# Kernel tuning notes

Hardware: AMD Instinct MI355X
Metric: run time of the kernel (lower is better)

The kernel has to match this reference:

```python
import jax, jax.numpy as jnp
import numpy as np

ODE_UNFOLDS = 6
EPS = 1e-8


def setup_inputs() -> dict:
    key = jax.random.key(0)
    ks = jax.random.split(key, 16)
    B, T, IN, U = 256, 128, 64, 256

    def unif(k, shape, lo, hi):
        return jax.random.uniform(k, shape, jnp.float32, lo, hi)

    def pm1(k, shape):  # random +/-1 reversal potentials (as in ncps erev init)
        return (2.0 * jax.random.bernoulli(k, 0.5, shape) - 1.0).astype(jnp.float32)

    return {
        "x_ltc": jax.random.normal(ks[0], (B, T, IN), jnp.float32),
        "timespans": jnp.ones((B, T, 1), jnp.float32),
        # sensory synapses (input -> units)
        "sensory_mu": unif(ks[1], (IN, U), 0.3, 0.8),
        "sensory_sigma": unif(ks[2], (IN, U), 3.0, 8.0),
        "sensory_w": unif(ks[3], (IN, U), 0.001, 1.0),
        "sensory_erev": pm1(ks[4], (IN, U)),
        # recurrent synapses (units -> units)
        "mu": unif(ks[5], (U, U), 0.3, 0.8),
        "sigma": unif(ks[6], (U, U), 3.0, 8.0),
        "w": unif(ks[7], (U, U), 0.001, 1.0),
        "erev": pm1(ks[8], (U, U)),
        # per-neuron leak / capacitance
        "gleak": unif(ks[9], (U,), 0.001, 1.0),
        "vleak": unif(ks[10], (U,), -0.2, 0.2),
        "cm": unif(ks[11], (U,), 0.4, 0.6),
        # affine input / output mappings
        "input_w": jnp.ones((IN,), jnp.float32),
        "input_b": jnp.zeros((IN,), jnp.float32),
        "output_w": jnp.ones((U,), jnp.float32),
        "output_b": jnp.zeros((U,), jnp.float32),
        # head: Linear(hidden, 1)
        "head_w": jax.random.normal(ks[12], (1, U), jnp.float32) * 0.05,
        "head_b": jnp.zeros((1,), jnp.float32),
    }


def reference(x_ltc, timespans, sensory_mu, sensory_sigma, sensory_w, sensory_erev,
              mu, sigma, w, erev, gleak, vleak, cm,
              input_w, input_b, output_w, output_b, head_w, head_b):
    B = x_ltc.shape[0]
    U = gleak.shape[0]

    def gate(v, mu_, sigma_):
        # v: (B, pre) -> (B, pre, post) sigmoid activation
        return jax.nn.sigmoid(sigma_ * (v[:, :, None] - mu_))

    def cell(v, xt, elapsed):
        x = xt * input_w + input_b                              # (B, IN)
        s_act = sensory_w * gate(x, sensory_mu, sensory_sigma)  # (B, IN, U)
        w_num_s = jnp.sum(s_act * sensory_erev, axis=1)          # (B, U)
        w_den_s = jnp.sum(s_act, axis=1)                         # (B, U)
        cm_t = cm / (elapsed / ODE_UNFOLDS)                      # (B, U) via (B,1) bcast
        for _ in range(ODE_UNFOLDS):                             # semi-implicit Euler unfolds
            w_act = w * gate(v, mu, sigma)                       # (B, U, U)
            w_num = jnp.sum(w_act * erev, axis=1) + w_num_s
            w_den = jnp.sum(w_act, axis=1) + w_den_s
            num = cm_t * v + gleak * vleak + w_num
            den = cm_t + gleak + w_den
            v = num / (den + EPS)
        return v

    def step(v, inp):
        xt, el = inp
        return cell(v, xt, el), None

    v0 = jnp.zeros((B, U), x_ltc.dtype)
    xs = (jnp.swapaxes(x_ltc, 0, 1), jnp.swapaxes(timespans, 0, 1))  # (T,B,IN), (T,B,1)
    vT, _ = jax.lax.scan(step, v0, xs)
    h_out = vT * output_w + output_b                             # output mapping of last step
    return h_out @ head_w.T + head_b                             # (B, 1)
```

## Files before the change

### kernel.cpp

```cpp
#include <hip/hip_runtime.h>
#include <hip/hip_bf16.h>
#include <hip/hip_fp16.h>

#define LOG2E 1.4426950408889634f

constexpr int B_ = 256, T_ = 128, IN_ = 64, U_ = 256;
constexpr int UNFOLDS = 6;

constexpr size_t OFF_RCD = 0;
constexpr size_t OFF_RWS = 262144;
constexpr size_t OFF_SCD = 393216;
constexpr size_t OFF_SWS = 458752;
constexpr size_t OFF_ELF = 491520;
constexpr size_t OFF_VEC = 622592;

typedef _Float16 hv2 __attribute__((ext_vector_type(2)));

__device__ __forceinline__ float ldf(const void* p, int idx, bool isbf) {
  return isbf ? __bfloat162float(((const __hip_bfloat16*)p)[idx])
              : ((const float*)p)[idx];
}

__device__ __forceinline__ float fdot2f(__half2 a, __half2 b, float c) {
#if __has_builtin(__builtin_amdgcn_fdot2)
  return __builtin_amdgcn_fdot2(__builtin_bit_cast(hv2, a),
                                __builtin_bit_cast(hv2, b), c, false);
#else
  return c + __low2float(a) * __low2float(b) +
         __high2float(a) * __high2float(b);
#endif
}

__device__ __forceinline__ unsigned packpair(float lo, float hi) {
  return __builtin_bit_cast(unsigned, __builtin_amdgcn_cvt_pkrtz(lo, hi));
}

__global__ __launch_bounds__(256) void ltc_prep(
    const void* tspan, const void* smu, const void* ssigma, const void* sw,
    const void* serev, const void* mu, const void* sigma, const void* w,
    const void* erev, const void* gleak, const void* vleak, const void* cm,
    const void* inw, const void* inb, const void* outw, const void* outb,
    const void* headw, const void* headb, char* __restrict__ ws) {
  const bool isbf = (((const unsigned*)tspan)[0] == 0x3F803F80u);
  const int idx = blockIdx.x * blockDim.x + threadIdx.x;

  uint2*    rcd = (uint2*)(ws + OFF_RCD);
  unsigned* rws = (unsigned*)(ws + OFF_RWS);
  uint2*    scd = (uint2*)(ws + OFF_SCD);
  unsigned* sws = (unsigned*)(ws + OFF_SWS);
  float*    elf = (float*)(ws + OFF_ELF);
  float*    vec = (float*)(ws + OFF_VEC);

  if (idx < (U_ * U_) / 2) {
    const int j = idx & 255, P = idx >> 8;
    const int e0 = (2 * P) * U_ + j, e1 = (2 * P + 1) * U_ + j;
    float sg0 = ldf(sigma, e0, isbf), m0 = ldf(mu, e0, isbf);
    float w0  = ldf(w, e0, isbf),     er0 = ldf(erev, e0, isbf);
    float sg1 = ldf(sigma, e1, isbf), m1 = ldf(mu, e1, isbf);
    float w1  = ldf(w, e1, isbf),     er1 = ldf(erev, e1, isbf);
    __half2 C, D, W;
    C.x = __float2half_rn(sg0 * m0 * LOG2E);  C.y = __float2half_rn(sg1 * m1 * LOG2E);
    D.x = __float2half_rn(-sg0 * LOG2E);      D.y = __float2half_rn(-sg1 * LOG2E);
    W.x = __float2half_rn(w0 * er0);          W.y = __float2half_rn(w1 * er1);
    rcd[P * 256 + j] = make_uint2(__builtin_bit_cast(unsigned, C),
                                  __builtin_bit_cast(unsigned, D));
    rws[P * 256 + j] = __builtin_bit_cast(unsigned, W);
  }
  if (idx < (IN_ * U_) / 2) {
    const int j = idx & 255, P = idx >> 8;
    const int e0 = (2 * P) * U_ + j, e1 = (2 * P + 1) * U_ + j;
    float sg0 = ldf(ssigma, e0, isbf), m0 = ldf(smu, e0, isbf);
    float w0  = ldf(sw, e0, isbf),     er0 = ldf(serev, e0, isbf);
    float sg1 = ldf(ssigma, e1, isbf), m1 = ldf(smu, e1, isbf);
    float w1  = ldf(sw, e1, isbf),     er1 = ldf(serev, e1, isbf);
    __half2 C, D, W;
    C.x = __float2half_rn(sg0 * m0 * LOG2E);  C.y = __float2half_rn(sg1 * m1 * LOG2E);
    D.x = __float2half_rn(-sg0 * LOG2E);      D.y = __float2half_rn(-sg1 * LOG2E);
    W.x = __float2half_rn(w0 * er0);          W.y = __float2half_rn(w1 * er1);
    scd[P * 256 + j] = make_uint2(__builtin_bit_cast(unsigned, C),
                                  __builtin_bit_cast(unsigned, D));
    sws[P * 256 + j] = __builtin_bit_cast(unsigned, W);
  }
  if (idx < B_ * T_) elf[idx] = ldf(tspan, idx, isbf);
  if (idx < U_) {
    float gl = ldf(gleak, idx, isbf);
    float hw = ldf(headw, idx, isbf);
    vec[idx]        = gl;
    vec[256 + idx]  = gl * ldf(vleak, idx, isbf);
    vec[512 + idx]  = ldf(cm, idx, isbf);
    vec[768 + idx]  = ldf(outw, idx, isbf) * hw;
    vec[1024 + idx] = ldf(outb, idx, isbf) * hw;
  }
  if (idx < IN_) {
    vec[1280 + idx] = ldf(inw, idx, isbf);
    vec[1344 + idx] = ldf(inb, idx, isbf);
  }
  if (idx == 0) vec[1408] = ldf(headb, 0, isbf);
}

__device__ __forceinline__ void pairj(unsigned uC, unsigned uD, unsigned uW,
                                      unsigned uV, __half2 one2,
                                      float& n, float& d) {
  const __half2 C  = __builtin_bit_cast(__half2, uC);
  const __half2 D  = __builtin_bit_cast(__half2, uD);
  const __half2 W  = __builtin_bit_cast(__half2, uW);
  const __half2 Wa = __builtin_bit_cast(__half2, uW & 0x7fff7fffu);
  const __half2 vh = __builtin_bit_cast(__half2, uV);
  __half2 th = __hfma2(D, vh, C);
  __half2 eh = h2exp2(th);
  __half2 ph = __hadd2(eh, one2);
  __half2 rh = h2rcp(ph);
  n = fdot2f(W, rh, n);
  d = fdot2f(Wa, rh, d);
}

__global__ __launch_bounds__(1024) void ltc_main(
    const void* __restrict__ x_ltc, const void* __restrict__ tspan,
    const char* __restrict__ ws, void* __restrict__ out) {
  __shared__ uint2    s_cd[8192];
  __shared__ unsigned s_ws[8192];
  __shared__ float2 redA[4][257];
  __shared__ float2 redB[4][257];
  __shared__ float2 redS[4][257];
  __shared__ float v_sh[U_];
  __shared__ __attribute__((aligned(16))) unsigned vh_sh[U_ / 2];
  __shared__ unsigned xh_sh[2][IN_ / 2];
  __shared__ float red[1024];

  const bool isbf = (((const unsigned*)tspan)[0] == 0x3F803F80u);
  const int b   = blockIdx.x;
  const int tid = threadIdx.x;
  const int j   = tid & 255;
  const int gq  = tid >> 8;

  const uint2*    rcd2 = (const uint2*)(ws + OFF_RCD);
  const unsigned* rws1 = (const unsigned*)(ws + OFF_RWS);
  const uint2*    scd2 = (const uint2*)(ws + OFF_SCD);
  const unsigned* sws1 = (const unsigned*)(ws + OFF_SWS);
  const float*    elf  = (const float*)(ws + OFF_ELF);
  const float*    vec  = (const float*)(ws + OFF_VEC);

  for (int i = tid; i < 8192; i += 1024) { s_cd[i] = scd2[i]; s_ws[i] = sws1[i]; }

  float r_gl = 0.f, r_glvl = 0.f, r_cm6 = 0.f;
  if (tid < U_) {
    r_gl   = vec[tid];
    r_glvl = vec[256 + tid];
    r_cm6  = vec[512 + tid] * (float)UNFOLDS;
    v_sh[tid] = 0.f;
  }
  if (tid < U_ / 2) vh_sh[tid] = 0u;

  const int xl = tid - 768;
  float r_iw0 = 0.f, r_iw1 = 0.f, r_ib0 = 0.f, r_ib1 = 0.f;
  if (xl >= 0 && xl < IN_ / 2) {
    r_iw0 = vec[1280 + 2 * xl]; r_iw1 = vec[1280 + 2 * xl + 1];
    r_ib0 = vec[1344 + 2 * xl]; r_ib1 = vec[1344 + 2 * xl + 1];
    float x0 = ldf(x_ltc, (b * T_ + 0) * IN_ + 2 * xl, isbf);
    float x1 = ldf(x_ltc, (b * T_ + 0) * IN_ + 2 * xl + 1, isbf);
    xh_sh[0][xl] = packpair(fmaf(x0, r_iw0, r_ib0), fmaf(x1, r_iw1, r_ib1));
  }
  __syncthreads();

  __half2 one2;
  one2.x = __float2half_rn(1.0f);
  one2.y = one2.x;

  float SN = 0.f, SD = 0.f, cmt = 0.f;

#pragma unroll 1
  for (int t = 0; t < T_; ++t) {
    {
      const unsigned* xc = xh_sh[t & 1];
      float sn = 0.f, sd = 0.f;
#pragma unroll
      for (int m = 0; m < 8; ++m) {
        const int P = gq * 8 + m;
        uint2 cd = s_cd[P * 256 + j];
        pairj(cd.x, cd.y, s_ws[P * 256 + j], xc[P], one2, sn, sd);
      }
      redS[gq][j] = make_float2(sn, sd);
    }
    {
      const uint4* vh4 = (const uint4*)vh_sh;
      float n = 0.f, d = 0.f;
#pragma unroll
      for (int mm = 0; mm < 8; ++mm) {
        uint4 vv = vh4[gq * 8 + mm];
        const int e = (gq * 32 + mm * 4) * 256 + j;
        uint2 c0 = rcd2[e];           unsigned w0 = rws1[e];
        uint2 c1 = rcd2[e + 256];     unsigned w1 = rws1[e + 256];
        uint2 c2 = rcd2[e + 512];     unsigned w2 = rws1[e + 512];
        uint2 c3 = rcd2[e + 768];     unsigned w3 = rws1[e + 768];
        pairj(c0.x, c0.y, w0, vv.x, one2, n, d);
        pairj(c1.x, c1.y, w1, vv.y, one2, n, d);
        pairj(c2.x, c2.y, w2, vv.z, one2, n, d);
        pairj(c3.x, c3.y, w3, vv.w, one2, n, d);
      }
      redA[gq][j] = make_float2(n, d);
    }
    __syncthreads();

    if (tid < U_) {
      float2 s0 = redS[0][tid], s1 = redS[1][tid], s2 = redS[2][tid], s3 = redS[3][tid];
      SN = s0.x + s1.x + s2.x + s3.x;
      SD = s0.y + s1.y + s2.y + s3.y;
      float el = elf[b * T_ + t];
      cmt = r_cm6 * __builtin_amdgcn_rcpf(el);
      float2 a0 = redA[0][tid], a1 = redA[1][tid], a2 = redA[2][tid], a3 = redA[3][tid];
      float n = a0.x + a1.x + a2.x + a3.x + SN;
      float d = a0.y + a1.y + a2.y + a3.y + SD;
      float vj = v_sh[tid];
      float vnew = (fmaf(cmt, vj, r_glvl) + n) *
                   __builtin_amdgcn_rcpf(cmt + r_gl + d + 1e-8f);
      v_sh[tid] = vnew;
      float vo = __shfl_xor(vnew, 1);
      if ((tid & 1) == 0) vh_sh[tid >> 1] = packpair(vnew, vo);
    }
    __syncthreads();

#pragma unroll 1
    for (int u = 1; u < UNFOLDS; ++u) {
      float2 (*dst)[257] = (u & 1) ? redB : redA;
      {
        const uint4* vh4 = (const uint4*)vh_sh;
        float n = 0.f, d = 0.f;
#pragma unroll
        for (int mm = 0; mm < 8; ++mm) {
          uint4 vv = vh4[gq * 8 + mm];
          const int e = (gq * 32 + mm * 4) * 256 + j;
          uint2 c0 = rcd2[e];           unsigned w0 = rws1[e];
          uint2 c1 = rcd2[e + 256];     unsigned w1 = rws1[e + 256];
          uint2 c2 = rcd2[e + 512];     unsigned w2 = rws1[e + 512];
          uint2 c3 = rcd2[e + 768];     unsigned w3 = rws1[e + 768];
          pairj(c0.x, c0.y, w0, vv.x, one2, n, d);
          pairj(c1.x, c1.y, w1, vv.y, one2, n, d);
          pairj(c2.x, c2.y, w2, vv.z, one2, n, d);
          pairj(c3.x, c3.y, w3, vv.w, one2, n, d);
        }
        dst[gq][j] = make_float2(n, d);
      }
      if (u == UNFOLDS - 1 && xl >= 0 && xl < IN_ / 2 && t + 1 < T_) {
        float x0 = ldf(x_ltc, (b * T_ + t + 1) * IN_ + 2 * xl, isbf);
        float x1 = ldf(x_ltc, (b * T_ + t + 1) * IN_ + 2 * xl + 1, isbf);
        xh_sh[(t + 1) & 1][xl] =
            packpair(fmaf(x0, r_iw0, r_ib0), fmaf(x1, r_iw1, r_ib1));
      }
      __syncthreads();
      if (tid < U_) {
        float2 a0 = dst[0][tid], a1 = dst[1][tid], a2 = dst[2][tid], a3 = dst[3][tid];
        float n = a0.x + a1.x + a2.x + a3.x + SN;
        float d = a0.y + a1.y + a2.y + a3.y + SD;
        float vj = v_sh[tid];
        float vnew = (fmaf(cmt, vj, r_glvl) + n) *
                     __builtin_amdgcn_rcpf(cmt + r_gl + d + 1e-8f);
        v_sh[tid] = vnew;
        float vo = __shfl_xor(vnew, 1);
        if ((tid & 1) == 0) vh_sh[tid >> 1] = packpair(vnew, vo);
      }
      __syncthreads();
    }
  }

  float val = 0.f;
  if (tid < U_) val = fmaf(v_sh[tid], vec[768 + tid], vec[1024 + tid]);
  red[tid] = val;
  __syncthreads();
  for (int s = 512; s > 0; s >>= 1) {
    if (tid < s) red[tid] += red[tid + s];
    __syncthreads();
  }
  if (tid == 0) {
    float o = red[0] + vec[1408];
    if (isbf) ((__hip_bfloat16*)out)[b] = __float2bfloat16(o);
    else      ((float*)out)[b] = o;
  }
}

extern "C" void kernel_launch(void* const* d_in, const int* in_sizes, int n_in,
                              void* d_out, int out_size, void* d_ws, size_t ws_size,
                              hipStream_t stream) {
  (void)in_sizes; (void)n_in; (void)out_size; (void)ws_size;
  const void* x_ltc  = d_in[0];
  const void* tspan  = d_in[1];
  const void* smu    = d_in[2];
  const void* ssigma = d_in[3];
  const void* sw     = d_in[4];
  const void* serev  = d_in[5];
  const void* mu     = d_in[6];
  const void* sigma  = d_in[7];
  const void* w      = d_in[8];
  const void* erev   = d_in[9];
  const void* gleak  = d_in[10];
  const void* vleak  = d_in[11];
  const void* cmv    = d_in[12];
  const void* inw    = d_in[13];
  const void* inb    = d_in[14];
  const void* outw   = d_in[15];
  const void* outb   = d_in[16];
  const void* headw  = d_in[17];
  const void* headb  = d_in[18];

  ltc_prep<<<128, 256, 0, stream>>>(
      tspan, smu, ssigma, sw, serev, mu, sigma, w, erev,
      gleak, vleak, cmv, inw, inb, outw, outb, headw, headb, (char*)d_ws);

  ltc_main<<<B_, 1024, 0, stream>>>(x_ltc, tspan, (const char*)d_ws, d_out);
}
```

Measured before the change: 4.148 ms.

## Software-pipeline recurrent weight loads, double-buffer state, keep v in registers

The first ODE unfold is folded into the common unfold loop. The packed half-precision state buffer is double-buffered. All four thread groups redundantly recompute the per-neuron update and keep v in registers, which drops the v_sh shared array and the redB buffer. Recurrent coefficient and weight global loads are prefetched one iteration ahead, and elapsed times are staged in LDS. A min-blocks launch bound is added, which may force the compiler to limit registers and risks spills alongside the added prefetch registers.

```diff
diff --git a/kernel.cpp b/kernel.cpp
--- a/kernel.cpp
+++ b/kernel.cpp
@@ -114,17 +114,16 @@
   d = fdot2f(Wa, rh, d);
 }
 
-__global__ __launch_bounds__(1024) void ltc_main(
+__global__ __launch_bounds__(1024, 4) void ltc_main(
     const void* __restrict__ x_ltc, const void* __restrict__ tspan,
     const char* __restrict__ ws, void* __restrict__ out) {
   __shared__ uint2    s_cd[8192];
   __shared__ unsigned s_ws[8192];
   __shared__ float2 redA[4][257];
-  __shared__ float2 redB[4][257];
   __shared__ float2 redS[4][257];
-  __shared__ float v_sh[U_];
-  __shared__ __attribute__((aligned(16))) unsigned vh_sh[U_ / 2];
+  __shared__ __attribute__((aligned(16))) unsigned vh_sh[2][U_ / 2];
   __shared__ unsigned xh_sh[2][IN_ / 2];
+  __shared__ float el_sh[T_];
   __shared__ float red[1024];
 
   const bool isbf = (((const unsigned*)tspan)[0] == 0x3F803F80u);
@@ -142,14 +141,13 @@
 
   for (int i = tid; i < 8192; i += 1024) { s_cd[i] = scd2[i]; s_ws[i] = sws1[i]; }
 
-  float r_gl = 0.f, r_glvl = 0.f, r_cm6 = 0.f;
-  if (tid < U_) {
-    r_gl   = vec[tid];
-    r_glvl = vec[256 + tid];
-    r_cm6  = vec[512 + tid] * (float)UNFOLDS;
-    v_sh[tid] = 0.f;
-  }
-  if (tid < U_ / 2) vh_sh[tid] = 0u;
+  const float r_gl   = vec[j];
+  const float r_glvl = vec[256 + j];
+  const float r_cm6  = vec[512 + j] * (float)UNFOLDS;
+  float vj = 0.f;
+
+  if (tid < T_) el_sh[tid] = elf[b * T_ + tid];
+  if (tid < U_ / 2) vh_sh[0][tid] = 0u;
 
   const int xl = tid - 768;
   float r_iw0 = 0.f, r_iw1 = 0.f, r_ib0 = 0.f, r_ib1 = 0.f;
@@ -167,6 +165,7 @@
   one2.y = one2.x;
 
   float SN = 0.f, SD = 0.f, cmt = 0.f;
+  int cur = 0;
 
 #pragma unroll 1
   for (int t = 0; t < T_; ++t) {
@@ -181,64 +180,35 @@
       }
       redS[gq][j] = make_float2(sn, sd);
     }
-    {
-      const uint4* vh4 = (const uint4*)vh_sh;
-      float n = 0.f, d = 0.f;
-#pragma unroll
-      for (int mm = 0; mm < 8; ++mm) {
-        uint4 vv = vh4[gq * 8 + mm];
-        const int e = (gq * 32 + mm * 4) * 256 + j;
-        uint2 c0 = rcd2[e];           unsigned w0 = rws1[e];
-        uint2 c1 = rcd2[e + 256];     unsigned w1 = rws1[e + 256];
-        uint2 c2 = rcd2[e + 512];     unsigned w2 = rws1[e + 512];
-        uint2 c3 = rcd2[e + 768];     unsigned w3 = rws1[e + 768];
-        pairj(c0.x, c0.y, w0, vv.x, one2, n, d);
-        pairj(c1.x, c1.y, w1, vv.y, one2, n, d);
-        pairj(c2.x, c2.y, w2, vv.z, one2, n, d);
-        pairj(c3.x, c3.y, w3, vv.w, one2, n, d);
-      }
-      redA[gq][j] = make_float2(n, d);
-    }
-    __syncthreads();
-
-    if (tid < U_) {
-      float2 s0 = redS[0][tid], s1 = redS[1][tid], s2 = redS[2][tid], s3 = redS[3][tid];
-      SN = s0.x + s1.x + s2.x + s3.x;
-      SD = s0.y + s1.y + s2.y + s3.y;
-      float el = elf[b * T_ + t];
-      cmt = r_cm6 * __builtin_amdgcn_rcpf(el);
-      float2 a0 = redA[0][tid], a1 = redA[1][tid], a2 = redA[2][tid], a3 = redA[3][tid];
-      float n = a0.x + a1.x + a2.x + a3.x + SN;
-      float d = a0.y + a1.y + a2.y + a3.y + SD;
-      float vj = v_sh[tid];
-      float vnew = (fmaf(cmt, vj, r_glvl) + n) *
-                   __builtin_amdgcn_rcpf(cmt + r_gl + d + 1e-8f);
-      v_sh[tid] = vnew;
-      float vo = __shfl_xor(vnew, 1);
-      if ((tid & 1) == 0) vh_sh[tid >> 1] = packpair(vnew, vo);
-    }
-    __syncthreads();
 
 #pragma unroll 1
-    for (int u = 1; u < UNFOLDS; ++u) {
-      float2 (*dst)[257] = (u & 1) ? redB : redA;
+    for (int u = 0; u < UNFOLDS; ++u) {
       {
-        const uint4* vh4 = (const uint4*)vh_sh;
+        const uint4* vh4 = (const uint4*)vh_sh[cur];
         float n = 0.f, d = 0.f;
+        const int e0 = (gq * 32) * 256 + j;
+        uint2 pc0 = rcd2[e0],       pc1 = rcd2[e0 + 256];
+        uint2 pc2 = rcd2[e0 + 512], pc3 = rcd2[e0 + 768];
+        unsigned pw0 = rws1[e0],       pw1 = rws1[e0 + 256];
+        unsigned pw2 = rws1[e0 + 512], pw3 = rws1[e0 + 768];
 #pragma unroll
         for (int mm = 0; mm < 8; ++mm) {
+          uint2 c0 = pc0, c1 = pc1, c2 = pc2, c3 = pc3;
+          unsigned w0 = pw0, w1 = pw1, w2 = pw2, w3 = pw3;
+          if (mm < 7) {
+            const int e = (gq * 32 + (mm + 1) * 4) * 256 + j;
+            pc0 = rcd2[e];       pc1 = rcd2[e + 256];
+            pc2 = rcd2[e + 512]; pc3 = rcd2[e + 768];
+            pw0 = rws1[e];       pw1 = rws1[e + 256];
+            pw2 = rws1[e + 512]; pw3 = rws1[e + 768];
+          }
           uint4 vv = vh4[gq * 8 + mm];
-          const int e = (gq * 32 + mm * 4) * 256 + j;
-          uint2 c0 = rcd2[e];           unsigned w0 = rws1[e];
-          uint2 c1 = rcd2[e + 256];     unsigned w1 = rws1[e + 256];
-          uint2 c2 = rcd2[e + 512];     unsigned w2 = rws1[e + 512];
-          uint2 c3 = rcd2[e + 768];     unsigned w3 = rws1[e + 768];
           pairj(c0.x, c0.y, w0, vv.x, one2, n, d);
           pairj(c1.x, c1.y, w1, vv.y, one2, n, d);
           pairj(c2.x, c2.y, w2, vv.z, one2, n, d);
           pairj(c3.x, c3.y, w3, vv.w, one2, n, d);
         }
-        dst[gq][j] = make_float2(n, d);
+        redA[gq][j] = make_float2(n, d);
       }
       if (u == UNFOLDS - 1 && xl >= 0 && xl < IN_ / 2 && t + 1 < T_) {
         float x0 = ldf(x_ltc, (b * T_ + t + 1) * IN_ + 2 * xl, isbf);
@@ -247,23 +217,31 @@
             packpair(fmaf(x0, r_iw0, r_ib0), fmaf(x1, r_iw1, r_ib1));
       }
       __syncthreads();
-      if (tid < U_) {
-        float2 a0 = dst[0][tid], a1 = dst[1][tid], a2 = dst[2][tid], a3 = dst[3][tid];
+
+      if (u == 0) {
+        float2 s0 = redS[0][j], s1 = redS[1][j], s2 = redS[2][j], s3 = redS[3][j];
+        SN = s0.x + s1.x + s2.x + s3.x;
+        SD = s0.y + s1.y + s2.y + s3.y;
+        cmt = r_cm6 * __builtin_amdgcn_rcpf(el_sh[t]);
+      }
+      {
+        float2 a0 = redA[0][j], a1 = redA[1][j], a2 = redA[2][j], a3 = redA[3][j];
         float n = a0.x + a1.x + a2.x + a3.x + SN;
         float d = a0.y + a1.y + a2.y + a3.y + SD;
-        float vj = v_sh[tid];
         float vnew = (fmaf(cmt, vj, r_glvl) + n) *
                      __builtin_amdgcn_rcpf(cmt + r_gl + d + 1e-8f);
-        v_sh[tid] = vnew;
+        vj = vnew;
         float vo = __shfl_xor(vnew, 1);
-        if ((tid & 1) == 0) vh_sh[tid >> 1] = packpair(vnew, vo);
+        if (tid < U_ && (tid & 1) == 0)
+          vh_sh[cur ^ 1][tid >> 1] = packpair(vnew, vo);
       }
       __syncthreads();
+      cur ^= 1;
     }
   }
 
   float val = 0.f;
-  if (tid < U_) val = fmaf(v_sh[tid], vec[768 + tid], vec[1024 + tid]);
+  if (tid < U_) val = fmaf(vj, vec[768 + tid], vec[1024 + tid]);
   red[tid] = val;
   __syncthreads();
   for (int s = 512; s > 0; s >>= 1) {
```

Measured after the change: 3.919 ms. -5.5%, faster.
